# Kernel optimization log

Measured on AMD Instinct MI355X. Metric: run time of the kernel, lower is better.

The kernel has to match this reference:

```python
import jax, jax.numpy as jnp
import numpy as np

TEMP = 0.1
TEMP_SUP = 0.5
PROP = 0.5  # proportion_pure_contrastive
SIGMA = 1.0
GAMMA = 1.0 / (2.0 * SIGMA ** 2)
INF = 1e8


def _l2norm(x, eps=1e-12):
    # torch F.normalize: x / max(||x||, eps)
    n = jnp.sqrt(jnp.sum(x * x, axis=-1, keepdims=True))
    return x / jnp.maximum(n, eps)


def _cross_entropy(logits, targets):
    # mean over rows of -log_softmax(logits)[i, targets[i]]
    logp = jax.nn.log_softmax(logits, axis=-1)
    return -jnp.mean(jnp.take_along_axis(logp, targets[:, None], axis=-1))


def setup_inputs() -> dict:
    key = jax.random.key(0)
    k1, k2, k3 = jax.random.split(key, 3)
    N, D = 4096, 256
    z_i = jax.random.normal(k1, (N, D), dtype=jnp.float32)
    z_j = jax.random.normal(k2, (N, D), dtype=jnp.float32)
    labels = jax.random.normal(k3, (N, 1), dtype=jnp.float32)
    return {"z_i": z_i, "z_j": z_j, "labels": labels}


def _forward(z_i, z_j, labels):
    N = z_i.shape[0]
    eye = jnp.eye(N, dtype=z_i.dtype)
    zin = _l2norm(z_i)
    zjn = _l2norm(z_j)

    # ---- pure contrastive branch (temperature TEMP) ----
    sim_zii = zin @ zin.T / TEMP - INF * eye
    sim_zjj = zjn @ zjn.T / TEMP - INF * eye
    sim_zij = zin @ zjn.T / TEMP
    correct = jnp.arange(N, dtype=jnp.int32)
    loss_i = _cross_entropy(jnp.concatenate([sim_zij, sim_zii], axis=1), correct)
    loss_j = _cross_entropy(jnp.concatenate([sim_zij.T, sim_zjj], axis=1), correct)
    loss_pure = loss_i + loss_j

    # ---- supervised branch (temperature TEMP_SUP) ----
    s_zii = zin @ zin.T / TEMP_SUP - INF * eye
    s_zjj = zjn @ zjn.T / TEMP_SUP - INF * eye
    s_zij = zin @ zjn.T / TEMP_SUP

    # RBF kernel on duplicated labels (detached in original -> stop_gradient)
    all_lab = jnp.tile(labels.reshape(N, -1), (2, 1))  # [2N, L]
    all_lab = jax.lax.stop_gradient(all_lab)
    sq = jnp.sum(all_lab * all_lab, axis=1)
    d2 = sq[:, None] + sq[None, :] - 2.0 * (all_lab @ all_lab.T)
    weights = jnp.exp(-GAMMA * jnp.maximum(d2, 0.0))  # [2N, 2N]
    weights = weights * (1.0 - jnp.eye(2 * N, dtype=weights.dtype))
    norm = jnp.sum(weights, axis=1, keepdims=True)  # [2N, 1]
    weights = weights / norm
    weights_norm = weights * jnp.log(norm)

    sim_Z = jnp.concatenate([
        jnp.concatenate([s_zii, s_zij], axis=1),
        jnp.concatenate([s_zij.T, s_zjj], axis=1),
    ], axis=0)  # [2N, 2N]
    log_sim_Z = jax.nn.log_softmax(sim_Z, axis=1)
    loss_sup = (-1.0 / N) * jnp.sum(weights * log_sim_Z)
    loss_sup += (-1.0 / N) * jnp.sum(weights_norm)

    return PROP * loss_pure + (1.0 - PROP) * loss_sup


def reference(z_i, z_j, labels):
    return _forward(z_i, z_j, labels)
```

## Files before the change

kernel.cpp:

```cpp
#include <hip/hip_runtime.h>
#include <hip/hip_bf16.h>

#define NN 4096
#define DD 256
#define CCN 8
#define TPB 16
#define LOG2E 1.44269504088896f

typedef __attribute__((ext_vector_type(8))) short bf16x8;
typedef __attribute__((ext_vector_type(4))) float f32x4;
typedef __attribute__((ext_vector_type(2))) float f32x2;

typedef const unsigned int __attribute__((address_space(1)))* gu32p;
typedef unsigned int __attribute__((address_space(3)))* su32p;

__device__ __forceinline__ float fexp2(float x) { return __builtin_amdgcn_exp2f(x); }

__global__ __launch_bounds__(256) void k_norm(const float* __restrict__ zi,
                                              const float* __restrict__ zj,
                                              const float* __restrict__ labels,
                                              __hip_bfloat16* __restrict__ oi,
                                              __hip_bfloat16* __restrict__ oj,
                                              float* __restrict__ T,
                                              float* __restrict__ out) {
  if (blockIdx.x == 0 && threadIdx.x == 0) out[0] = 0.f;
  int gw = (blockIdx.x * 256 + threadIdx.x) >> 6;
  int lane = threadIdx.x & 63;
  int wave = threadIdx.x >> 6;
  const float* src = (gw < NN) ? zi : zj;
  __hip_bfloat16* dst = (gw < NN) ? oi : oj;
  int row = (gw < NN) ? gw : gw - NN;
  float4 v = ((const float4*)(src + (size_t)row * DD))[lane];
  float ss = v.x * v.x + v.y * v.y + v.z * v.z + v.w * v.w;
#pragma unroll
  for (int m = 1; m < 64; m <<= 1) ss += __shfl_xor(ss, m);
  float s = 1.0f / fmaxf(sqrtf(ss), 1e-12f);
  __hip_bfloat16* d = dst + (size_t)row * DD + lane * 4;
  d[0] = __float2bfloat16(v.x * s);
  d[1] = __float2bfloat16(v.y * s);
  d[2] = __float2bfloat16(v.z * s);
  d[3] = __float2bfloat16(v.w * s);

  if (wave < 2) {
    int r = blockIdx.x * 2 + wave;
    float lr = labels[r];
    float acc = 0.f;
    for (int it = 0; it < NN / 64; ++it) {
      float dl = lr - labels[it * 64 + lane];
      acc += fexp2(dl * dl * (-0.5f * LOG2E));
    }
#pragma unroll
    for (int m = 1; m < 64; m <<= 1) acc += __shfl_xor(acc, m);
    if (lane == 0) T[r] = acc;
  }
}

template <int MODE, bool COL>
__device__ __forceinline__ void epi(
    const f32x4 acc[2][2], const f32x2 labr[2][2], const float* __restrict__ labels,
    f32x2 rA[2][2], f32x2 rB[2][2], f32x2 rC[2][2],
    f32x2 cw2[2][3], float* __restrict__ diag,
    int rowbase, int colbase, int wave, int fr, int kg) {
#pragma unroll
  for (int cf = 0; cf < 2; ++cf) {
    const int cg = colbase + cf * 16 + fr;
    const float labc = labels[cg];
    const f32x2 labc2 = {labc, labc};
#pragma unroll
    for (int sub = 0; sub < 2; ++sub) {
#pragma unroll
      for (int pp = 0; pp < 2; ++pp) {
        f32x2 S = {acc[sub][cf][2 * pp], acc[sub][cf][2 * pp + 1]};
        f32x2 arg = S * (2.f * LOG2E) + (-2.f * LOG2E);
        f32x2 b;
        b.x = fexp2(arg.x);
        b.y = fexp2(arg.y);
        f32x2 b2 = b * b;
        f32x2 b5 = b2 * b2 * b;
        f32x2 dl = labr[sub][pp] - labc2;
        f32x2 e = (dl * (-0.5f * LOG2E)) * dl;
        f32x2 kk;
        kk.x = fexp2(e.x);
        kk.y = fexp2(e.y);
        f32x2 ks = kk * S;
        if (MODE != 0) {
          const int rg = rowbase + wave * 32 + sub * 16 + kg * 4 + 2 * pp;
          if (MODE == 1) {
            if (rg == cg) diag[cg] = S.x;
            if (rg + 1 == cg) diag[cg] = S.y;
          } else {
            if (rg == cg)     { b5.x = 0.f; b.x = 0.f; ks.x = 0.f; }
            if (rg + 1 == cg) { b5.y = 0.f; b.y = 0.f; ks.y = 0.f; }
          }
        }
        rA[sub][pp] += b5;
        rB[sub][pp] += b;
        rC[sub][pp] += ks;
        if (COL) {
          cw2[cf][0] += b5;
          cw2[cf][1] += b;
          cw2[cf][2] += ks;
        }
      }
    }
  }
}

__global__ __launch_bounds__(256, 2) void k_main(
    const __hip_bfloat16* __restrict__ zin, const __hip_bfloat16* __restrict__ zjn,
    const float* __restrict__ labels,
    float* __restrict__ part, float* __restrict__ colp, float* __restrict__ diag) {
  __shared__ short lB[2][32 * 256];

  const int cc = blockIdx.x;
  const int by = blockIdx.y;
  const int combo = blockIdx.z;
  const bool COLF = (combo == 0);

  const __hip_bfloat16* Ap = (combo == 2) ? zjn : zin;
  const __hip_bfloat16* Bp = (combo == 1) ? zin : zjn;

  const int tid = threadIdx.x;
  const int lane = tid & 63;
  const int wave = tid >> 6;
  const int fr = lane & 15;
  const int kg = lane >> 4;
  const int rowbase = by * 128;
  char* lBc = (char*)lB;

  bf16x8 a[2][8];
#pragma unroll
  for (int sub = 0; sub < 2; ++sub) {
    const __hip_bfloat16* Ar =
        Ap + (size_t)(rowbase + wave * 32 + sub * 16 + fr) * DD + kg * 8;
#pragma unroll
    for (int k = 0; k < 8; ++k) a[sub][k] = *(const bf16x8*)(Ar + k * 32);
  }

  f32x2 labr[2][2];
#pragma unroll
  for (int sub = 0; sub < 2; ++sub)
#pragma unroll
    for (int pp = 0; pp < 2; ++pp) {
      const float* lp = labels + rowbase + wave * 32 + sub * 16 + kg * 4 + 2 * pp;
      labr[sub][pp] = (f32x2){lp[0], lp[1]};
    }

  f32x2 rA[2][2] = {}, rB[2][2] = {}, rC[2][2] = {};

  const int frb = (fr >> 2) & 1;
  const int P0 = fr * 512 + ((kg ^ (fr & 3)) << 4) + (frb << 6);

#define STAGE(t, buf)                                                         \
  {                                                                           \
    const char* Bt = (const char*)Bp + (size_t)(cc * 512 + (t) * 32) * 512;   \
    char* dst = lBc + (buf) * 16384;                                          \
    _Pragma("unroll") for (int j = 0; j < 4; ++j) {                           \
      int f = tid + 256 * j;                                                  \
      int g = f ^ ((f >> 5) & 7);                                             \
      __builtin_amdgcn_global_load_lds(                                       \
          (gu32p)(const void*)(Bt + (size_t)g * 16),                          \
          (su32p)(void*)(dst + (wave * 64 + 256 * j) * 16), 16, 0, 0);        \
    }                                                                         \
  }

  auto do_mfma = [&](f32x4 (&ACC)[2][2], const char* cur) {
#pragma unroll
    for (int s2 = 0; s2 < 2; ++s2)
#pragma unroll
      for (int cf = 0; cf < 2; ++cf) ACC[s2][cf] = (f32x4){0.f, 0.f, 0.f, 0.f};
#pragma unroll
    for (int k = 0; k < 8; ++k) {
      const char* bbase = cur + (P0 ^ (k << 6));
#pragma unroll
      for (int cf = 0; cf < 2; ++cf) {
        bf16x8 bv = *(const bf16x8*)(bbase + cf * 8192);
        ACC[0][cf] = __builtin_amdgcn_mfma_f32_16x16x32_bf16(a[0][k], bv, ACC[0][cf], 0, 0, 0);
        ACC[1][cf] = __builtin_amdgcn_mfma_f32_16x16x32_bf16(a[1][k], bv, ACC[1][cf], 0, 0, 0);
      }
    }
  };

  auto do_epi = [&](const f32x4 (&ACC)[2][2], int te) {
    const int colbase = cc * 512 + te * 32;
    const unsigned dtt = (unsigned)(te + 16 * cc - 4 * by);
    f32x2 cw2[2][3] = {};
    if (COLF) {
      if (dtt < 4u)
        epi<1, true>(ACC, labr, labels, rA, rB, rC, cw2, diag, rowbase, colbase, wave, fr, kg);
      else
        epi<0, true>(ACC, labr, labels, rA, rB, rC, cw2, diag, rowbase, colbase, wave, fr, kg);
      float* cp = colp + ((size_t)(by * 128 + cc * TPB + te) * 4 + wave) * 96;
#pragma unroll
      for (int cf = 0; cf < 2; ++cf)
#pragma unroll
        for (int p = 0; p < 3; ++p) {
          float v = cw2[cf][p].x + cw2[cf][p].y;
          v += __shfl_xor(v, 16);
          v += __shfl_xor(v, 32);
          if (kg == 0) cp[p * 32 + cf * 16 + fr] = v;
        }
    } else {
      if (dtt < 4u)
        epi<2, false>(ACC, labr, labels, rA, rB, rC, cw2, diag, rowbase, colbase, wave, fr, kg);
      else
        epi<0, false>(ACC, labr, labels, rA, rB, rC, cw2, diag, rowbase, colbase, wave, fr, kg);
    }
  };

  f32x4 accA[2][2], accB[2][2];

  STAGE(0, 0);
  __syncthreads();

#pragma unroll
  for (int tt = 0; tt < TPB / 2; ++tt) {
    const int t0 = 2 * tt, t1 = 2 * tt + 1;
    STAGE(t0 + 1, 1);
    if (t0 > 0) do_epi(accB, t0 - 1);
    do_mfma(accA, lBc);
    __syncthreads();

    if (t1 < TPB - 1) STAGE(t1 + 1, 0);
    do_epi(accA, t0);
    do_mfma(accB, lBc + 16384);
    __syncthreads();
  }
  do_epi(accB, TPB - 1);

  float* pc = part + (size_t)cc * 9 * NN;
  const int pr = combo;
#pragma unroll
  for (int sub = 0; sub < 2; ++sub)
#pragma unroll
    for (int pp = 0; pp < 2; ++pp)
#pragma unroll
      for (int comp = 0; comp < 2; ++comp) {
        float va = rA[sub][pp][comp], vb = rB[sub][pp][comp], vc = rC[sub][pp][comp];
#pragma unroll
        for (int m = 1; m < 16; m <<= 1) {
          va += __shfl_xor(va, m);
          vb += __shfl_xor(vb, m);
          vc += __shfl_xor(vc, m);
        }
        if (fr == 0) {
          int r = rowbase + wave * 32 + sub * 16 + kg * 4 + 2 * pp + comp;
          pc[pr * NN + r] = va;
          pc[(3 + pr) * NN + r] = vb;
          pc[(6 + pr) * NN + r] = vc;
        }
      }
}

__global__ __launch_bounds__(256) void k_final(
    const float* __restrict__ part, const float* __restrict__ colp,
    const float* __restrict__ diag, const float* __restrict__ T,
    float* __restrict__ out) {
  int r = blockIdx.x * 256 + threadIdx.x;
  float st[9];
#pragma unroll
  for (int p = 0; p < 9; ++p) {
    float s = 0.f;
#pragma unroll
    for (int c = 0; c < CCN; ++c) s += part[((size_t)c * 9 + p) * NN + r];
    st[p] = s;
  }
  float a3 = 0.f, b3 = 0.f, c3 = 0.f;
  const int cct = r >> 5, c31 = r & 31;
  for (int by = 0; by < 32; ++by) {
    const float* cp = colp + (size_t)(by * 128 + cct) * 4 * 96;
#pragma unroll
    for (int w = 0; w < 4; ++w) {
      a3 += cp[w * 96 + c31];
      b3 += cp[w * 96 + 32 + c31];
      c3 += cp[w * 96 + 64 + c31];
    }
  }
  float d = diag[r];
  float accP = logf(st[0] + st[1]) + logf(a3 + st[2]) + 20.f - 20.f * d;
  float nrm = 2.f * T[r] - 1.f;
  float W = 2.f * (st[6] + st[7] + c3 + st[8]) / nrm;
  float accS = logf(st[3] + st[4]) + logf(b3 + st[5]) + 4.f - W - 2.f * logf(nrm);
  float v = accP + accS;
#pragma unroll
  for (int m = 1; m < 64; m <<= 1) v += __shfl_xor(v, m);
  __shared__ float red[4];
  if ((threadIdx.x & 63) == 0) red[threadIdx.x >> 6] = v;
  __syncthreads();
  if (threadIdx.x == 0)
    atomicAdd(out, 0.5f * (red[0] + red[1] + red[2] + red[3]) / (float)NN);
}

extern "C" void kernel_launch(void* const* d_in, const int* in_sizes, int n_in,
                              void* d_out, int out_size, void* d_ws, size_t ws_size,
                              hipStream_t stream) {
  const float* zi = (const float*)d_in[0];
  const float* zj = (const float*)d_in[1];
  const float* labels = (const float*)d_in[2];
  float* out = (float*)d_out;

  char* ws = (char*)d_ws;
  __hip_bfloat16* zinH = (__hip_bfloat16*)ws;
  __hip_bfloat16* zjnH = (__hip_bfloat16*)(ws + (size_t)NN * DD * 2);
  float* part = (float*)(ws + (size_t)NN * DD * 4);
  float* colp = part + (size_t)CCN * 9 * NN;
  float* diag = colp + (size_t)4096 * 4 * 96;
  float* T = diag + NN;

  k_norm<<<2 * NN / 4, 256, 0, stream>>>(zi, zj, labels, zinH, zjnH, T, out);

  dim3 grid(CCN, NN / 128, 3);
  k_main<<<grid, 256, 0, stream>>>(zinH, zjnH, labels, part, colp, diag);

  k_final<<<NN / 256, 256, 0, stream>>>(part, colp, diag, T, out);
}
```

Before: 73.86 us.

## Exploit symmetry of self-similarity blocks to skip lower-triangle tiles

For the zi·ziᵀ and zj·zjᵀ combos, each block now skips column tiles strictly below the diagonal. It computes only the upper triangle, masks entries with cg<=rg in diagonal tiles, and emits column partial sums for every combo, so the skipped lower half is rebuilt from the column sums in the final kernel. This cuts roughly a third of the MFMA and exp work but brings unbalanced block lengths and a runtime-bounded loop that is no longer fully unrolled. It also triples the colp workspace and adds column reductions in k_final.

Result: slower. 98.14 us (+32.9%).

```diff
diff --git a/kernel.cpp b/kernel.cpp
--- a/kernel.cpp
+++ b/kernel.cpp
@@ -6,6 +6,7 @@
 #define CCN 8
 #define TPB 16
 #define LOG2E 1.44269504088896f
+#define COLPSZ ((size_t)4096 * 4 * 96)
 
 typedef __attribute__((ext_vector_type(8))) short bf16x8;
 typedef __attribute__((ext_vector_type(4))) float f32x4;
@@ -55,7 +56,7 @@
   }
 }
 
-template <int MODE, bool COL>
+template <int MODE>
 __device__ __forceinline__ void epi(
     const f32x4 acc[2][2], const f32x2 labr[2][2], const float* __restrict__ labels,
     f32x2 rA[2][2], f32x2 rB[2][2], f32x2 rC[2][2],
@@ -89,18 +90,16 @@
             if (rg == cg) diag[cg] = S.x;
             if (rg + 1 == cg) diag[cg] = S.y;
           } else {
-            if (rg == cg)     { b5.x = 0.f; b.x = 0.f; ks.x = 0.f; }
-            if (rg + 1 == cg) { b5.y = 0.f; b.y = 0.f; ks.y = 0.f; }
+            if (cg <= rg)     { b5.x = 0.f; b.x = 0.f; ks.x = 0.f; }
+            if (cg <= rg + 1) { b5.y = 0.f; b.y = 0.f; ks.y = 0.f; }
           }
         }
         rA[sub][pp] += b5;
         rB[sub][pp] += b;
         rC[sub][pp] += ks;
-        if (COL) {
-          cw2[cf][0] += b5;
-          cw2[cf][1] += b;
-          cw2[cf][2] += ks;
-        }
+        cw2[cf][0] += b5;
+        cw2[cf][1] += b;
+        cw2[cf][2] += ks;
       }
     }
   }
@@ -115,7 +114,6 @@
   const int cc = blockIdx.x;
   const int by = blockIdx.y;
   const int combo = blockIdx.z;
-  const bool COLF = (combo == 0);
 
   const __hip_bfloat16* Ap = (combo == 2) ? zjn : zin;
   const __hip_bfloat16* Bp = (combo == 1) ? zin : zjn;
@@ -128,28 +126,33 @@
   const int rowbase = by * 128;
   char* lBc = (char*)lB;
 
-  bf16x8 a[2][8];
-#pragma unroll
-  for (int sub = 0; sub < 2; ++sub) {
-    const __hip_bfloat16* Ar =
-        Ap + (size_t)(rowbase + wave * 32 + sub * 16 + fr) * DD + kg * 8;
-#pragma unroll
-    for (int k = 0; k < 8; ++k) a[sub][k] = *(const bf16x8*)(Ar + k * 32);
-  }
-
-  f32x2 labr[2][2];
-#pragma unroll
-  for (int sub = 0; sub < 2; ++sub)
-#pragma unroll
-    for (int pp = 0; pp < 2; ++pp) {
-      const float* lp = labels + rowbase + wave * 32 + sub * 16 + kg * 4 + 2 * pp;
-      labr[sub][pp] = (f32x2){lp[0], lp[1]};
-    }
-
   f32x2 rA[2][2] = {}, rB[2][2] = {}, rC[2][2] = {};
 
-  const int frb = (fr >> 2) & 1;
-  const int P0 = fr * 512 + ((kg ^ (fr & 3)) << 4) + (frb << 6);
+  int tstart = 0;
+  if (combo != 0) tstart = max(0, 4 * by - 16 * cc);
+  const int nt = TPB - tstart;
+
+  if (nt > 0) {
+    bf16x8 a[2][8];
+#pragma unroll
+    for (int sub = 0; sub < 2; ++sub) {
+      const __hip_bfloat16* Ar =
+          Ap + (size_t)(rowbase + wave * 32 + sub * 16 + fr) * DD + kg * 8;
+#pragma unroll
+      for (int k = 0; k < 8; ++k) a[sub][k] = *(const bf16x8*)(Ar + k * 32);
+    }
+
+    f32x2 labr[2][2];
+#pragma unroll
+    for (int sub = 0; sub < 2; ++sub)
+#pragma unroll
+      for (int pp = 0; pp < 2; ++pp) {
+        const float* lp = labels + rowbase + wave * 32 + sub * 16 + kg * 4 + 2 * pp;
+        labr[sub][pp] = (f32x2){lp[0], lp[1]};
+      }
+
+    const int frb = (fr >> 2) & 1;
+    const int P0 = fr * 512 + ((kg ^ (fr & 3)) << 4) + (frb << 6);
 
 #define STAGE(t, buf)                                                         \
   {                                                                           \
@@ -164,33 +167,37 @@
     }                                                                         \
   }
 
-  auto do_mfma = [&](f32x4 (&ACC)[2][2], const char* cur) {
-#pragma unroll
-    for (int s2 = 0; s2 < 2; ++s2)
-#pragma unroll
-      for (int cf = 0; cf < 2; ++cf) ACC[s2][cf] = (f32x4){0.f, 0.f, 0.f, 0.f};
-#pragma unroll
-    for (int k = 0; k < 8; ++k) {
-      const char* bbase = cur + (P0 ^ (k << 6));
-#pragma unroll
-      for (int cf = 0; cf < 2; ++cf) {
-        bf16x8 bv = *(const bf16x8*)(bbase + cf * 8192);
-        ACC[0][cf] = __builtin_amdgcn_mfma_f32_16x16x32_bf16(a[0][k], bv, ACC[0][cf], 0, 0, 0);
-        ACC[1][cf] = __builtin_amdgcn_mfma_f32_16x16x32_bf16(a[1][k], bv, ACC[1][cf], 0, 0, 0);
-      }
-    }
-  };
-
-  auto do_epi = [&](const f32x4 (&ACC)[2][2], int te) {
-    const int colbase = cc * 512 + te * 32;
-    const unsigned dtt = (unsigned)(te + 16 * cc - 4 * by);
-    f32x2 cw2[2][3] = {};
-    if (COLF) {
-      if (dtt < 4u)
-        epi<1, true>(ACC, labr, labels, rA, rB, rC, cw2, diag, rowbase, colbase, wave, fr, kg);
-      else
-        epi<0, true>(ACC, labr, labels, rA, rB, rC, cw2, diag, rowbase, colbase, wave, fr, kg);
-      float* cp = colp + ((size_t)(by * 128 + cc * TPB + te) * 4 + wave) * 96;
+    auto do_mfma = [&](f32x4 (&ACC)[2][2], const char* cur) {
+#pragma unroll
+      for (int s2 = 0; s2 < 2; ++s2)
+#pragma unroll
+        for (int cf = 0; cf < 2; ++cf) ACC[s2][cf] = (f32x4){0.f, 0.f, 0.f, 0.f};
+#pragma unroll
+      for (int k = 0; k < 8; ++k) {
+        const char* bbase = cur + (P0 ^ (k << 6));
+#pragma unroll
+        for (int cf = 0; cf < 2; ++cf) {
+          bf16x8 bv = *(const bf16x8*)(bbase + cf * 8192);
+          ACC[0][cf] = __builtin_amdgcn_mfma_f32_16x16x32_bf16(a[0][k], bv, ACC[0][cf], 0, 0, 0);
+          ACC[1][cf] = __builtin_amdgcn_mfma_f32_16x16x32_bf16(a[1][k], bv, ACC[1][cf], 0, 0, 0);
+        }
+      }
+    };
+
+    auto do_epi = [&](const f32x4 (&ACC)[2][2], int te) {
+      const int colbase = cc * 512 + te * 32;
+      const unsigned dtt = (unsigned)(te + 16 * cc - 4 * by);
+      f32x2 cw2[2][3] = {};
+      if (dtt < 4u) {
+        if (combo == 0)
+          epi<1>(ACC, labr, labels, rA, rB, rC, cw2, diag, rowbase, colbase, wave, fr, kg);
+        else
+          epi<2>(ACC, labr, labels, rA, rB, rC, cw2, diag, rowbase, colbase, wave, fr, kg);
+      } else {
+        epi<0>(ACC, labr, labels, rA, rB, rC, cw2, diag, rowbase, colbase, wave, fr, kg);
+      }
+      float* cp = colp + (size_t)combo * COLPSZ +
+                  ((size_t)(by * 128 + cc * TPB + te) * 4 + wave) * 96;
 #pragma unroll
       for (int cf = 0; cf < 2; ++cf)
 #pragma unroll
@@ -200,33 +207,27 @@
           v += __shfl_xor(v, 32);
           if (kg == 0) cp[p * 32 + cf * 16 + fr] = v;
         }
-    } else {
-      if (dtt < 4u)
-        epi<2, false>(ACC, labr, labels, rA, rB, rC, cw2, diag, rowbase, colbase, wave, fr, kg);
-      else
-        epi<0, false>(ACC, labr, labels, rA, rB, rC, cw2, diag, rowbase, colbase, wave, fr, kg);
-    }
-  };
-
-  f32x4 accA[2][2], accB[2][2];
-
-  STAGE(0, 0);
-  __syncthreads();
-
-#pragma unroll
-  for (int tt = 0; tt < TPB / 2; ++tt) {
-    const int t0 = 2 * tt, t1 = 2 * tt + 1;
-    STAGE(t0 + 1, 1);
-    if (t0 > 0) do_epi(accB, t0 - 1);
-    do_mfma(accA, lBc);
+    };
+
+    f32x4 accA[2][2], accB[2][2];
+
+    STAGE(tstart, 0);
     __syncthreads();
 
-    if (t1 < TPB - 1) STAGE(t1 + 1, 0);
-    do_epi(accA, t0);
-    do_mfma(accB, lBc + 16384);
-    __syncthreads();
-  }
-  do_epi(accB, TPB - 1);
+    for (int tt = 0; tt < nt / 2; ++tt) {
+      const int t0 = tstart + 2 * tt, t1 = t0 + 1;
+      STAGE(t0 + 1, 1);
+      if (t0 > tstart) do_epi(accB, t0 - 1);
+      do_mfma(accA, lBc);
+      __syncthreads();
+
+      if (t1 < TPB - 1) STAGE(t1 + 1, 0);
+      do_epi(accA, t0);
+      do_mfma(accB, lBc + 16384);
+      __syncthreads();
+    }
+    do_epi(accB, TPB - 1);
+  }
 
   float* pc = part + (size_t)cc * 9 * NN;
   const int pr = combo;
@@ -265,8 +266,8 @@
     for (int c = 0; c < CCN; ++c) s += part[((size_t)c * 9 + p) * NN + r];
     st[p] = s;
   }
+  const int cct = r >> 5, c31 = r & 31;
   float a3 = 0.f, b3 = 0.f, c3 = 0.f;
-  const int cct = r >> 5, c31 = r & 31;
   for (int by = 0; by < 32; ++by) {
     const float* cp = colp + (size_t)(by * 128 + cct) * 4 * 96;
 #pragma unroll
@@ -276,11 +277,28 @@
       c3 += cp[w * 96 + 64 + c31];
     }
   }
+  float a2 = 0.f, b2 = 0.f, c2 = 0.f, a4 = 0.f, b4 = 0.f, c4 = 0.f;
+  const int bymax = cct >> 2;
+  for (int by = 0; by <= bymax; ++by) {
+    const float* cp1 = colp + COLPSZ + (size_t)(by * 128 + cct) * 4 * 96;
+    const float* cp2 = colp + 2 * COLPSZ + (size_t)(by * 128 + cct) * 4 * 96;
+#pragma unroll
+    for (int w = 0; w < 4; ++w) {
+      a2 += cp1[w * 96 + c31];
+      b2 += cp1[w * 96 + 32 + c31];
+      c2 += cp1[w * 96 + 64 + c31];
+      a4 += cp2[w * 96 + c31];
+      b4 += cp2[w * 96 + 32 + c31];
+      c4 += cp2[w * 96 + 64 + c31];
+    }
+  }
+  float A2 = st[1] + a2, B2 = st[4] + b2, C2 = st[7] + c2;
+  float A4 = st[2] + a4, B4 = st[5] + b4, C4 = st[8] + c4;
   float d = diag[r];
-  float accP = logf(st[0] + st[1]) + logf(a3 + st[2]) + 20.f - 20.f * d;
+  float accP = logf(st[0] + A2) + logf(a3 + A4) + 20.f - 20.f * d;
   float nrm = 2.f * T[r] - 1.f;
-  float W = 2.f * (st[6] + st[7] + c3 + st[8]) / nrm;
-  float accS = logf(st[3] + st[4]) + logf(b3 + st[5]) + 4.f - W - 2.f * logf(nrm);
+  float W = 2.f * (st[6] + C2 + c3 + C4) / nrm;
+  float accS = logf(st[3] + B2) + logf(b3 + B4) + 4.f - W - 2.f * logf(nrm);
   float v = accP + accS;
 #pragma unroll
   for (int m = 1; m < 64; m <<= 1) v += __shfl_xor(v, m);
@@ -304,7 +322,7 @@
   __hip_bfloat16* zjnH = (__hip_bfloat16*)(ws + (size_t)NN * DD * 2);
   float* part = (float*)(ws + (size_t)NN * DD * 4);
   float* colp = part + (size_t)CCN * 9 * NN;
-  float* diag = colp + (size_t)4096 * 4 * 96;
+  float* diag = colp + 3 * COLPSZ;
   float* T = diag + NN;
 
   k_norm<<<2 * NN / 4, 256, 0, stream>>>(zi, zj, labels, zinH, zjnH, T, out);
```

## Split label-kernel and final-reduction work across more waves; raise MFMA priority

Applied to the files above, without the earlier changes.

The RBF row-sum in k_norm is now split across all four waves, two per label row, and combined through shared memory instead of leaving two waves idle. k_final launches 4x more blocks and gives each row four threads, each summing a quarter of the column partials, combined with shuffles. s_setprio is raised around the MFMA sections in k_main so matrix work gets issue priority over the epilogue in other waves. The aim is shorter serial tails in the small kernels and better MFMA/epilogue overlap, at the cost of an extra barrier and redundant partial-sum loads in k_final.

Result: no change. 73.34 us (-0.7%).

```diff
diff --git a/kernel.cpp b/kernel.cpp
--- a/kernel.cpp
+++ b/kernel.cpp
@@ -23,6 +23,7 @@
                                               __hip_bfloat16* __restrict__ oj,
                                               float* __restrict__ T,
                                               float* __restrict__ out) {
+  __shared__ float Tred[2][2];
   if (blockIdx.x == 0 && threadIdx.x == 0) out[0] = 0.f;
   int gw = (blockIdx.x * 256 + threadIdx.x) >> 6;
   int lane = threadIdx.x & 63;
@@ -41,18 +42,22 @@
   d[2] = __float2bfloat16(v.z * s);
   d[3] = __float2bfloat16(v.w * s);
 
-  if (wave < 2) {
-    int r = blockIdx.x * 2 + wave;
+  {
+    int r = blockIdx.x * 2 + (wave & 1);
+    int h = wave >> 1;
     float lr = labels[r];
     float acc = 0.f;
-    for (int it = 0; it < NN / 64; ++it) {
+    for (int it = h * 32; it < h * 32 + 32; ++it) {
       float dl = lr - labels[it * 64 + lane];
       acc += fexp2(dl * dl * (-0.5f * LOG2E));
     }
 #pragma unroll
     for (int m = 1; m < 64; m <<= 1) acc += __shfl_xor(acc, m);
-    if (lane == 0) T[r] = acc;
-  }
+    if (lane == 0) Tred[wave & 1][h] = acc;
+  }
+  __syncthreads();
+  if (threadIdx.x < 2)
+    T[blockIdx.x * 2 + threadIdx.x] = Tred[threadIdx.x][0] + Tred[threadIdx.x][1];
 }
 
 template <int MODE, bool COL>
@@ -218,12 +223,16 @@
     const int t0 = 2 * tt, t1 = 2 * tt + 1;
     STAGE(t0 + 1, 1);
     if (t0 > 0) do_epi(accB, t0 - 1);
+    __builtin_amdgcn_s_setprio(1);
     do_mfma(accA, lBc);
+    __builtin_amdgcn_s_setprio(0);
     __syncthreads();
 
     if (t1 < TPB - 1) STAGE(t1 + 1, 0);
     do_epi(accA, t0);
+    __builtin_amdgcn_s_setprio(1);
     do_mfma(accB, lBc + 16384);
+    __builtin_amdgcn_s_setprio(0);
     __syncthreads();
   }
   do_epi(accB, TPB - 1);
@@ -256,7 +265,8 @@
     const float* __restrict__ part, const float* __restrict__ colp,
     const float* __restrict__ diag, const float* __restrict__ T,
     float* __restrict__ out) {
-  int r = blockIdx.x * 256 + threadIdx.x;
+  int r = blockIdx.x * 64 + (threadIdx.x >> 2);
+  int q = threadIdx.x & 3;
   float st[9];
 #pragma unroll
   for (int p = 0; p < 9; ++p) {
@@ -267,7 +277,7 @@
   }
   float a3 = 0.f, b3 = 0.f, c3 = 0.f;
   const int cct = r >> 5, c31 = r & 31;
-  for (int by = 0; by < 32; ++by) {
+  for (int by = 8 * q; by < 8 * q + 8; ++by) {
     const float* cp = colp + (size_t)(by * 128 + cct) * 4 * 96;
 #pragma unroll
     for (int w = 0; w < 4; ++w) {
@@ -276,12 +286,19 @@
       c3 += cp[w * 96 + 64 + c31];
     }
   }
-  float d = diag[r];
-  float accP = logf(st[0] + st[1]) + logf(a3 + st[2]) + 20.f - 20.f * d;
-  float nrm = 2.f * T[r] - 1.f;
-  float W = 2.f * (st[6] + st[7] + c3 + st[8]) / nrm;
-  float accS = logf(st[3] + st[4]) + logf(b3 + st[5]) + 4.f - W - 2.f * logf(nrm);
-  float v = accP + accS;
+  a3 += __shfl_xor(a3, 1); a3 += __shfl_xor(a3, 2);
+  b3 += __shfl_xor(b3, 1); b3 += __shfl_xor(b3, 2);
+  c3 += __shfl_xor(c3, 1); c3 += __shfl_xor(c3, 2);
+
+  float v = 0.f;
+  if (q == 0) {
+    float d = diag[r];
+    float accP = logf(st[0] + st[1]) + logf(a3 + st[2]) + 20.f - 20.f * d;
+    float nrm = 2.f * T[r] - 1.f;
+    float W = 2.f * (st[6] + st[7] + c3 + st[8]) / nrm;
+    float accS = logf(st[3] + st[4]) + logf(b3 + st[5]) + 4.f - W - 2.f * logf(nrm);
+    v = accP + accS;
+  }
 #pragma unroll
   for (int m = 1; m < 64; m <<= 1) v += __shfl_xor(v, m);
   __shared__ float red[4];
@@ -312,5 +329,5 @@
   dim3 grid(CCN, NN / 128, 3);
   k_main<<<grid, 256, 0, stream>>>(zinH, zjnH, labels, part, colp, diag);
 
-  k_final<<<NN / 256, 256, 0, stream>>>(part, colp, diag, T, out);
-}
+  k_final<<<NN / 64, 256, 0, stream>>>(part, colp, diag, T, out);
+}
```
